# Kernel tuning notes

Hardware: AMD Instinct MI355X
Metric: run time of the kernel (lower is better)

The kernel has to match this reference:

```python
import jax, jax.numpy as jnp
import numpy as np

REG_LAMBDA = 0.1   # registration_lambda
EPS = 1e-8         # kornia convert_points_from_homogeneous eps


def angle_axis_to_rotation_matrix(aa):
    # aa: [B,3] angle-axis -> [B,3,3] rotation via Rodrigues formula
    theta2 = jnp.sum(aa * aa, axis=-1)                      # [B]
    theta = jnp.sqrt(theta2 + 1e-12)
    wx, wy, wz = aa[:, 0], aa[:, 1], aa[:, 2]
    z = jnp.zeros_like(wx)
    K = jnp.stack([z, -wz, wy, wz, z, -wx, -wy, wx, z], axis=-1).reshape(-1, 3, 3)
    A = (jnp.sin(theta) / theta)[:, None, None]
    B = ((1.0 - jnp.cos(theta)) / (theta2 + 1e-12))[:, None, None]
    I = jnp.eye(3, dtype=aa.dtype)
    return I + A * K + B * (K @ K)


def generate_transformation(position, angle):
    # [B,3],[B,3] -> [B,4,4] SE(3)
    R = angle_axis_to_rotation_matrix(angle)
    b = position.shape[0]
    top = jnp.concatenate([R, position[:, :, None]], axis=2)                      # [B,3,4]
    bottom = jnp.broadcast_to(jnp.array([0., 0., 0., 1.], dtype=position.dtype), (b, 1, 4))
    return jnp.concatenate([top, bottom], axis=1)


def generate_relative_transformation(pos_a, ang_a, pos_b, ang_b):
    Ta = generate_transformation(pos_a, ang_a)
    Tb = generate_transformation(pos_b, ang_b)
    return jnp.linalg.inv(Tb) @ Ta


def grid_sample_bilinear_zeros(img, xn, yn):
    # img: [B,C,H,W]; xn,yn: [B,H,W] in [-1,1]; align_corners=True, zeros padding
    B, C, H, W = img.shape
    ix = (xn + 1.0) * (W - 1) * 0.5
    iy = (yn + 1.0) * (H - 1) * 0.5
    x0 = jnp.floor(ix)
    y0 = jnp.floor(iy)
    wx1 = ix - x0
    wy1 = iy - y0

    def tap(xf, yf, w):
        valid = (xf >= 0) & (xf <= W - 1) & (yf >= 0) & (yf <= H - 1)
        xi = jnp.clip(xf, 0, W - 1).astype(jnp.int32)
        yi = jnp.clip(yf, 0, H - 1).astype(jnp.int32)
        vals = jax.vmap(lambda im, yy, xx: im[:, yy, xx])(img, yi, xi)  # [B,C,H,W]
        return vals * (w * valid)[:, None, :, :]

    return (tap(x0, y0, (1 - wx1) * (1 - wy1))
            + tap(x0 + 1, y0, wx1 * (1 - wy1))
            + tap(x0, y0 + 1, (1 - wx1) * wy1)
            + tap(x0 + 1, y0 + 1, wx1 * wy1))


def warp_frame_depth(image_src, depth_dst, src_trans_dst, K):
    # kornia.geometry.depth.warp_frame_depth
    B, C, H, W = image_src.shape
    u = jnp.arange(W, dtype=image_src.dtype)
    v = jnp.arange(H, dtype=image_src.dtype)
    uu, vv = jnp.meshgrid(u, v, indexing='xy')               # each [H,W]
    pix = jnp.stack([uu, vv, jnp.ones_like(uu)], axis=0)     # [3,H,W]
    rays = jnp.einsum('ij,jhw->ihw', jnp.linalg.inv(K), pix)  # unproject directions
    pts_dst = depth_dst * rays[None]                         # [B,3,H,W] 3D points in dst frame
    R = src_trans_dst[:, :3, :3]
    t = src_trans_dst[:, :3, 3]
    pts_src = jnp.einsum('bij,bjhw->bihw', R, pts_dst) + t[:, :, None, None]
    proj = jnp.einsum('ij,bjhw->bihw', K, pts_src)           # project to src pixels
    z = proj[:, 2]
    scale = jnp.where(jnp.abs(z) > EPS, 1.0 / z, jnp.ones_like(z))
    x = proj[:, 0] * scale
    y = proj[:, 1] * scale
    xn = 2.0 * x / (W - 1) - 1.0                             # normalize_pixel_coordinates
    yn = 2.0 * y / (H - 1) - 1.0
    return grid_sample_bilinear_zeros(image_src, xn, yn)


def setup_inputs() -> dict:
    key = jax.random.key(0)
    ks = jax.random.split(key, 6)
    B, H, W = 16, 384, 1280
    current_depth = jax.random.uniform(ks[0], (B, 1, H, W), jnp.float32) * 50.0 + 1.0
    next_depth = jax.random.uniform(ks[1], (B, 1, H, W), jnp.float32) * 50.0 + 1.0
    current_position = jax.random.normal(ks[2], (B, 3), jnp.float32) * 0.5
    next_position = jax.random.normal(ks[3], (B, 3), jnp.float32) * 0.5
    current_angle = jax.random.normal(ks[4], (B, 3), jnp.float32) * 0.05
    next_angle = jax.random.normal(ks[5], (B, 3), jnp.float32) * 0.05
    camera_matrix = jnp.array([[707.0912, 0.0, 640.0],
                               [0.0, 707.0912, 192.0],
                               [0.0, 0.0, 1.0]], dtype=jnp.float32)
    return {"current_depth": current_depth, "next_depth": next_depth,
            "current_position": current_position, "next_position": next_position,
            "current_angle": current_angle, "next_angle": next_angle,
            "camera_matrix": camera_matrix}


def reference(current_depth, next_depth, current_position, next_position,
              current_angle, next_angle, camera_matrix):
    T_c2n = generate_relative_transformation(current_position, current_angle,
                                             next_position, next_angle)
    T_n2c = generate_relative_transformation(next_position, next_angle,
                                             current_position, current_angle)
    generated_next_depth = warp_frame_depth(current_depth, next_depth, T_n2c, camera_matrix)
    generated_current_depth = warp_frame_depth(next_depth, current_depth, T_c2n, camera_matrix)
    loss_previous = jnp.mean(jnp.abs(generated_current_depth - current_depth))
    loss_next = jnp.mean(jnp.abs(generated_next_depth - next_depth))
    return (loss_previous + loss_next) / 2.0 * REG_LAMBDA
```

## Files before the change

kernel.cpp:

```cpp
#include <hip/hip_runtime.h>
#include <math.h>

constexpr int B = 16, H = 384, W = 1280;
constexpr int HW = H * W;
constexpr int NPIX = B * HW;
constexpr int HW4 = HW / 4;
constexpr int W4 = W / 4;
constexpr int NBLOCKS = 2048;
constexpr int NTHREADS = 256;
constexpr int NXCD = 8;
constexpr int BLK_PER_XCD = NBLOCKS / NXCD;
constexpr int THR_PER_XCD = BLK_PER_XCD * NTHREADS;
constexpr float EPSV = 1e-8f;

constexpr int PARAMS_FLOATS = B * 24;

__device__ inline void aa_to_R(float x, float y, float z, float R[9]) {
    float t2 = x * x + y * y + z * z;
    float th = sqrtf(t2 + 1e-12f);
    float A = sinf(th) / th;
    float Bc = (1.0f - cosf(th)) / (t2 + 1e-12f);
    R[0] = 1.0f + Bc * (-(y * y + z * z));
    R[1] = A * (-z) + Bc * (x * y);
    R[2] = A * ( y) + Bc * (x * z);
    R[3] = A * ( z) + Bc * (x * y);
    R[4] = 1.0f + Bc * (-(x * x + z * z));
    R[5] = A * (-x) + Bc * (y * z);
    R[6] = A * (-y) + Bc * (x * z);
    R[7] = A * ( x) + Bc * (y * z);
    R[8] = 1.0f + Bc * (-(x * x + y * y));
}

__device__ inline void mat3_mul(const float* A, const float* Bm, float* C) {
#pragma unroll
    for (int i = 0; i < 3; i++)
#pragma unroll
        for (int j = 0; j < 3; j++)
            C[i * 3 + j] = A[i * 3 + 0] * Bm[0 * 3 + j]
                         + A[i * 3 + 1] * Bm[1 * 3 + j]
                         + A[i * 3 + 2] * Bm[2 * 3 + j];
}

__device__ inline void compute_dir(const float Ra[9], const float Rb[9],
                                   const float ta[3], const float tb[3],
                                   const float K[9], const float Ki[9],
                                   float* out) {
    float Rrel[9];
#pragma unroll
    for (int i = 0; i < 3; i++)
#pragma unroll
        for (int j = 0; j < 3; j++)
            Rrel[i * 3 + j] = Ra[0 * 3 + i] * Rb[0 * 3 + j]
                            + Ra[1 * 3 + i] * Rb[1 * 3 + j]
                            + Ra[2 * 3 + i] * Rb[2 * 3 + j];
    float dt[3] = { tb[0] - ta[0], tb[1] - ta[1], tb[2] - ta[2] };
    float trel[3];
#pragma unroll
    for (int i = 0; i < 3; i++)
        trel[i] = Ra[0 * 3 + i] * dt[0] + Ra[1 * 3 + i] * dt[1] + Ra[2 * 3 + i] * dt[2];
    float tmp[9], M[9];
    mat3_mul(Rrel, Ki, tmp);
    mat3_mul(K, tmp, M);
#pragma unroll
    for (int i = 0; i < 9; i++) out[i] = M[i];
#pragma unroll
    for (int i = 0; i < 3; i++)
        out[9 + i] = K[i * 3 + 0] * trel[0] + K[i * 3 + 1] * trel[1] + K[i * 3 + 2] * trel[2];
}

__global__ void grl_setup_kernel(const float* __restrict__ cpos, const float* __restrict__ npos,
                                 const float* __restrict__ cang, const float* __restrict__ nang,
                                 const float* __restrict__ Kmat, float* __restrict__ ws) {
    int b = threadIdx.x;
    if (b >= B) return;
    float Rc[9], Rn[9];
    aa_to_R(cang[3 * b + 0], cang[3 * b + 1], cang[3 * b + 2], Rc);
    aa_to_R(nang[3 * b + 0], nang[3 * b + 1], nang[3 * b + 2], Rn);
    float tc[3] = { cpos[3 * b + 0], cpos[3 * b + 1], cpos[3 * b + 2] };
    float tn[3] = { npos[3 * b + 0], npos[3 * b + 1], npos[3 * b + 2] };
    float K[9];
#pragma unroll
    for (int i = 0; i < 9; i++) K[i] = Kmat[i];
    float det = K[0] * (K[4] * K[8] - K[5] * K[7])
              - K[1] * (K[3] * K[8] - K[5] * K[6])
              + K[2] * (K[3] * K[7] - K[4] * K[6]);
    float id = 1.0f / det;
    float Ki[9] = {
        (K[4] * K[8] - K[5] * K[7]) * id, (K[2] * K[7] - K[1] * K[8]) * id, (K[1] * K[5] - K[2] * K[4]) * id,
        (K[5] * K[6] - K[3] * K[8]) * id, (K[0] * K[8] - K[2] * K[6]) * id, (K[2] * K[3] - K[0] * K[5]) * id,
        (K[3] * K[7] - K[4] * K[6]) * id, (K[1] * K[6] - K[0] * K[7]) * id, (K[0] * K[4] - K[1] * K[3]) * id };
    float* out = ws + b * 24;
    compute_dir(Rc, Rn, tc, tn, K, Ki, out);
    compute_dir(Rn, Rc, tn, tc, K, Ki, out + 12);
}

__device__ inline float2 load2u(const float* __restrict__ p) {
    float2 v;
    __builtin_memcpy(&v, p, sizeof(float2));
    return v;
}

__global__ __launch_bounds__(NTHREADS, 4) void grl_warp_loss_kernel(
        const float* __restrict__ cur, const float* __restrict__ nxt,
        const float* __restrict__ ws, float* __restrict__ partials) {
    int bid = blockIdx.x;
    int xcd = bid & (NXCD - 1);
    int j   = bid >> 3;
    int tid0 = j * NTHREADS + (int)threadIdx.x;
    float sum = 0.0f;

    for (int bb = 0; bb < 2; ++bb) {
        int b = xcd * 2 + bb;
        const float* __restrict__ prm = ws + b * 24;
        float M[2][9], kt[2][3];
#pragma unroll
        for (int i = 0; i < 9; i++) { M[0][i] = prm[i]; M[1][i] = prm[12 + i]; }
#pragma unroll
        for (int i = 0; i < 3; i++) { kt[0][i] = prm[9 + i]; kt[1][i] = prm[21 + i]; }
        const float* __restrict__ srcimg[2];
        srcimg[0] = cur + b * HW;
        srcimg[1] = nxt + b * HW;

        for (int idx = tid0; idx < HW4; idx += THR_PER_XCD) {
            int h  = idx / W4;
            int w4 = idx - h * W4;
            int p  = idx * 4;
            const float4 c4 = *(const float4*)(srcimg[0] + p);
            const float4 n4 = *(const float4*)(srcimg[1] + p);
            float fh = (float)h;
            float dst[2][4] = { { n4.x, n4.y, n4.z, n4.w },
                                { c4.x, c4.y, c4.z, c4.w } };

            float2 pv[2][4][2];
            float  mxl[2][4], mxr[2][4];
            float  myt[2][4], myb[2][4];
            int    sL[2][4], sR[2][4];

#pragma unroll
            for (int dir = 0; dir < 2; dir++) {
                float rx = M[dir][1] * fh + M[dir][2];
                float ry = M[dir][4] * fh + M[dir][5];
                float rz = M[dir][7] * fh + M[dir][8];
#pragma unroll
                for (int k = 0; k < 4; k++) {
                    float fw = (float)(w4 * 4 + k);
                    float d  = dst[dir][k];
                    float px = d * (M[dir][0] * fw + rx) + kt[dir][0];
                    float py = d * (M[dir][3] * fw + ry) + kt[dir][1];
                    float pz = d * (M[dir][6] * fw + rz) + kt[dir][2];
                    float scale = (fabsf(pz) > EPSV) ? (1.0f / pz) : 1.0f;
                    float ix = px * scale, iy = py * scale;
                    float x0f = floorf(ix), y0f = floorf(iy);
                    float wx1 = ix - x0f, wy1 = iy - y0f;
                    float wx0 = 1.0f - wx1, wy0 = 1.0f - wy1;
                    bool vx0 = (x0f >= 0.0f)        & (x0f <= (float)(W - 1));
                    bool vx1 = (x0f + 1.0f >= 0.0f) & (x0f + 1.0f <= (float)(W - 1));
                    bool vy0 = (y0f >= 0.0f)        & (y0f <= (float)(H - 1));
                    bool vy1 = (y0f + 1.0f >= 0.0f) & (y0f + 1.0f <= (float)(H - 1));
                    mxl[dir][k] = vx0 ? wx0 : 0.0f;
                    mxr[dir][k] = vx1 ? wx1 : 0.0f;
                    myt[dir][k] = vy0 ? wy0 : 0.0f;
                    myb[dir][k] = vy1 ? wy1 : 0.0f;
                    int xi0 = (int)fminf(fmaxf(x0f,        0.0f), (float)(W - 1));
                    int xi1 = (int)fminf(fmaxf(x0f + 1.0f, 0.0f), (float)(W - 1));
                    int yi0 = (int)fminf(fmaxf(y0f,        0.0f), (float)(H - 1));
                    int yi1 = (int)fminf(fmaxf(y0f + 1.0f, 0.0f), (float)(H - 1));
                    int xp  = min(xi0, W - 2);
                    sL[dir][k] = xi0 - xp;
                    sR[dir][k] = xi1 - xp;
                    pv[dir][k][0] = load2u(srcimg[dir] + yi0 * W + xp);
                    pv[dir][k][1] = load2u(srcimg[dir] + yi1 * W + xp);
                }
            }
            __builtin_amdgcn_sched_barrier(0);
#pragma unroll
            for (int dir = 0; dir < 2; dir++)
#pragma unroll
                for (int k = 0; k < 4; k++) {
                    float2 p0 = pv[dir][k][0], p1 = pv[dir][k][1];
                    float v00 = sL[dir][k] ? p0.y : p0.x;
                    float v01 = sR[dir][k] ? p0.y : p0.x;
                    float v10 = sL[dir][k] ? p1.y : p1.x;
                    float v11 = sR[dir][k] ? p1.y : p1.x;
                    float acc = (v00 * mxl[dir][k] + v01 * mxr[dir][k]) * myt[dir][k]
                              + (v10 * mxl[dir][k] + v11 * mxr[dir][k]) * myb[dir][k];
                    sum += fabsf(acc - dst[dir][k]);
                }
        }
    }

#pragma unroll
    for (int off2 = 32; off2 > 0; off2 >>= 1) sum += __shfl_down(sum, off2, 64);
    __shared__ float smem[NTHREADS / 64];
    int lane = threadIdx.x & 63, wid = threadIdx.x >> 6;
    if (lane == 0) smem[wid] = sum;
    __syncthreads();
    if (threadIdx.x == 0) {
        float t = 0.0f;
#pragma unroll
        for (int i = 0; i < NTHREADS / 64; i++) t += smem[i];
        partials[blockIdx.x] = t;
    }
}

__global__ __launch_bounds__(256) void grl_finalize_kernel(const float* __restrict__ partials,
                                                           float* __restrict__ out) {
    float sum = 0.0f;
    for (int i = threadIdx.x; i < NBLOCKS; i += 256) sum += partials[i];
#pragma unroll
    for (int off = 32; off > 0; off >>= 1) sum += __shfl_down(sum, off, 64);
    __shared__ float smem[4];
    int lane = threadIdx.x & 63, wid = threadIdx.x >> 6;
    if (lane == 0) smem[wid] = sum;
    __syncthreads();
    if (threadIdx.x == 0) {
        float t = smem[0] + smem[1] + smem[2] + smem[3];
        out[0] = t * (0.1f / (2.0f * (float)NPIX));
    }
}

extern "C" void kernel_launch(void* const* d_in, const int* in_sizes, int n_in,
                              void* d_out, int out_size, void* d_ws, size_t ws_size,
                              hipStream_t stream) {
    const float* cur  = (const float*)d_in[0];
    const float* nxt  = (const float*)d_in[1];
    const float* cpos = (const float*)d_in[2];
    const float* npos = (const float*)d_in[3];
    const float* cang = (const float*)d_in[4];
    const float* nang = (const float*)d_in[5];
    const float* Kmat = (const float*)d_in[6];
    float* ws = (float*)d_ws;
    float* partials = ws + PARAMS_FLOATS;

    grl_setup_kernel<<<1, 64, 0, stream>>>(cpos, npos, cang, nang, Kmat, ws);
    grl_warp_loss_kernel<<<NBLOCKS, NTHREADS, 0, stream>>>(cur, nxt, ws, partials);
    grl_finalize_kernel<<<1, 256, 0, stream>>>(partials, (float*)d_out);
}
```

Baseline: 116.9 us.

## Software-pipeline gather loads across flattened tasks with two in-flight stages

Merges the two per-XCD batch loops into one flat task space and unrolls it into a fixed sequence of issue/consume stages, so one stage's gather loads are outstanding while the previous stage is reduced. The bilinear x-select is folded into four precomputed tap coefficients, which removes the per-tap selects. Launch bounds drop to two blocks per SIMD to leave room for the doubled register staging. The trade-off is lower occupancy and an unrolled schedule that assumes at most four tasks per thread, which holds for the fixed sizes.

```diff
diff --git a/kernel.cpp b/kernel.cpp
--- a/kernel.cpp
+++ b/kernel.cpp
@@ -11,6 +11,7 @@
 constexpr int NXCD = 8;
 constexpr int BLK_PER_XCD = NBLOCKS / NXCD;
 constexpr int THR_PER_XCD = BLK_PER_XCD * NTHREADS;
+constexpr int NTASK = 2 * HW4;
 constexpr float EPSV = 1e-8f;
 
 constexpr int PARAMS_FLOATS = B * 24;
@@ -100,7 +101,92 @@
     return v;
 }
 
-__global__ __launch_bounds__(NTHREADS, 4) void grl_warp_loss_kernel(
+struct Stage {
+    float2 p0[8], p1[8];
+    float  c00[8], c01[8], c10[8], c11[8];
+    float  dst[8];
+};
+
+__device__ inline void issue_stage(int t, int xcd,
+                                   const float* __restrict__ cur,
+                                   const float* __restrict__ nxt,
+                                   const float* __restrict__ ws, Stage& S) {
+    int bl  = (t >= HW4) ? 1 : 0;
+    int idx = t - bl * HW4;
+    int b   = xcd * 2 + bl;
+    const float* __restrict__ prm = ws + b * 24;
+    const float* __restrict__ img0 = cur + b * HW;
+    const float* __restrict__ img1 = nxt + b * HW;
+    int h  = idx / W4;
+    int w4 = idx - h * W4;
+    int p  = idx * 4;
+    const float4 c4 = *(const float4*)(img0 + p);
+    const float4 n4 = *(const float4*)(img1 + p);
+    float fh = (float)h;
+    float dstv[2][4] = { { n4.x, n4.y, n4.z, n4.w },
+                         { c4.x, c4.y, c4.z, c4.w } };
+#pragma unroll
+    for (int dir = 0; dir < 2; dir++) {
+        const float* __restrict__ img = dir ? img1 : img0;
+        float M0 = prm[dir * 12 + 0], M1 = prm[dir * 12 + 1], M2 = prm[dir * 12 + 2];
+        float M3 = prm[dir * 12 + 3], M4 = prm[dir * 12 + 4], M5 = prm[dir * 12 + 5];
+        float M6 = prm[dir * 12 + 6], M7 = prm[dir * 12 + 7], M8 = prm[dir * 12 + 8];
+        float k0 = prm[dir * 12 + 9], k1 = prm[dir * 12 + 10], k2 = prm[dir * 12 + 11];
+        float rx = M1 * fh + M2;
+        float ry = M4 * fh + M5;
+        float rz = M7 * fh + M8;
+#pragma unroll
+        for (int k = 0; k < 4; k++) {
+            int i = dir * 4 + k;
+            float fw = (float)(w4 * 4 + k);
+            float d  = dstv[dir][k];
+            float px = d * (M0 * fw + rx) + k0;
+            float py = d * (M3 * fw + ry) + k1;
+            float pz = d * (M6 * fw + rz) + k2;
+            float scale = (fabsf(pz) > EPSV) ? (1.0f / pz) : 1.0f;
+            float ix = px * scale, iy = py * scale;
+            float x0f = floorf(ix), y0f = floorf(iy);
+            float wx1 = ix - x0f, wy1 = iy - y0f;
+            float wx0 = 1.0f - wx1, wy0 = 1.0f - wy1;
+            bool vx0 = (x0f >= 0.0f)        & (x0f <= (float)(W - 1));
+            bool vx1 = (x0f + 1.0f >= 0.0f) & (x0f + 1.0f <= (float)(W - 1));
+            bool vy0 = (y0f >= 0.0f)        & (y0f <= (float)(H - 1));
+            bool vy1 = (y0f + 1.0f >= 0.0f) & (y0f + 1.0f <= (float)(H - 1));
+            float mxl = vx0 ? wx0 : 0.0f;
+            float mxr = vx1 ? wx1 : 0.0f;
+            float myt = vy0 ? wy0 : 0.0f;
+            float myb = vy1 ? wy1 : 0.0f;
+            int xi0 = (int)fminf(fmaxf(x0f,        0.0f), (float)(W - 1));
+            int xi1 = (int)fminf(fmaxf(x0f + 1.0f, 0.0f), (float)(W - 1));
+            int yi0 = (int)fminf(fmaxf(y0f,        0.0f), (float)(H - 1));
+            int yi1 = (int)fminf(fmaxf(y0f + 1.0f, 0.0f), (float)(H - 1));
+            int xp  = min(xi0, W - 2);
+            int sL = xi0 - xp, sR = xi1 - xp;
+            float ax = (sL ? 0.0f : mxl) + (sR ? 0.0f : mxr);
+            float bx = (sL ? mxl : 0.0f) + (sR ? mxr : 0.0f);
+            S.c00[i] = ax * myt;
+            S.c01[i] = bx * myt;
+            S.c10[i] = ax * myb;
+            S.c11[i] = bx * myb;
+            S.dst[i] = d;
+            S.p0[i] = load2u(img + yi0 * W + xp);
+            S.p1[i] = load2u(img + yi1 * W + xp);
+        }
+    }
+}
+
+__device__ inline float consume_stage(const Stage& S) {
+    float s = 0.0f;
+#pragma unroll
+    for (int i = 0; i < 8; i++) {
+        float g = S.p0[i].x * S.c00[i] + S.p0[i].y * S.c01[i]
+                + S.p1[i].x * S.c10[i] + S.p1[i].y * S.c11[i];
+        s += fabsf(g - S.dst[i]);
+    }
+    return s;
+}
+
+__global__ __launch_bounds__(NTHREADS, 2) void grl_warp_loss_kernel(
         const float* __restrict__ cur, const float* __restrict__ nxt,
         const float* __restrict__ ws, float* __restrict__ partials) {
     int bid = blockIdx.x;
@@ -109,84 +195,22 @@
     int tid0 = j * NTHREADS + (int)threadIdx.x;
     float sum = 0.0f;
 
-    for (int bb = 0; bb < 2; ++bb) {
-        int b = xcd * 2 + bb;
-        const float* __restrict__ prm = ws + b * 24;
-        float M[2][9], kt[2][3];
-#pragma unroll
-        for (int i = 0; i < 9; i++) { M[0][i] = prm[i]; M[1][i] = prm[12 + i]; }
-#pragma unroll
-        for (int i = 0; i < 3; i++) { kt[0][i] = prm[9 + i]; kt[1][i] = prm[21 + i]; }
-        const float* __restrict__ srcimg[2];
-        srcimg[0] = cur + b * HW;
-        srcimg[1] = nxt + b * HW;
-
-        for (int idx = tid0; idx < HW4; idx += THR_PER_XCD) {
-            int h  = idx / W4;
-            int w4 = idx - h * W4;
-            int p  = idx * 4;
-            const float4 c4 = *(const float4*)(srcimg[0] + p);
-            const float4 n4 = *(const float4*)(srcimg[1] + p);
-            float fh = (float)h;
-            float dst[2][4] = { { n4.x, n4.y, n4.z, n4.w },
-                                { c4.x, c4.y, c4.z, c4.w } };
-
-            float2 pv[2][4][2];
-            float  mxl[2][4], mxr[2][4];
-            float  myt[2][4], myb[2][4];
-            int    sL[2][4], sR[2][4];
-
-#pragma unroll
-            for (int dir = 0; dir < 2; dir++) {
-                float rx = M[dir][1] * fh + M[dir][2];
-                float ry = M[dir][4] * fh + M[dir][5];
-                float rz = M[dir][7] * fh + M[dir][8];
-#pragma unroll
-                for (int k = 0; k < 4; k++) {
-                    float fw = (float)(w4 * 4 + k);
-                    float d  = dst[dir][k];
-                    float px = d * (M[dir][0] * fw + rx) + kt[dir][0];
-                    float py = d * (M[dir][3] * fw + ry) + kt[dir][1];
-                    float pz = d * (M[dir][6] * fw + rz) + kt[dir][2];
-                    float scale = (fabsf(pz) > EPSV) ? (1.0f / pz) : 1.0f;
-                    float ix = px * scale, iy = py * scale;
-                    float x0f = floorf(ix), y0f = floorf(iy);
-                    float wx1 = ix - x0f, wy1 = iy - y0f;
-                    float wx0 = 1.0f - wx1, wy0 = 1.0f - wy1;
-                    bool vx0 = (x0f >= 0.0f)        & (x0f <= (float)(W - 1));
-                    bool vx1 = (x0f + 1.0f >= 0.0f) & (x0f + 1.0f <= (float)(W - 1));
-                    bool vy0 = (y0f >= 0.0f)        & (y0f <= (float)(H - 1));
-                    bool vy1 = (y0f + 1.0f >= 0.0f) & (y0f + 1.0f <= (float)(H - 1));
-                    mxl[dir][k] = vx0 ? wx0 : 0.0f;
-                    mxr[dir][k] = vx1 ? wx1 : 0.0f;
-                    myt[dir][k] = vy0 ? wy0 : 0.0f;
-                    myb[dir][k] = vy1 ? wy1 : 0.0f;
-                    int xi0 = (int)fminf(fmaxf(x0f,        0.0f), (float)(W - 1));
-                    int xi1 = (int)fminf(fmaxf(x0f + 1.0f, 0.0f), (float)(W - 1));
-                    int yi0 = (int)fminf(fmaxf(y0f,        0.0f), (float)(H - 1));
-                    int yi1 = (int)fminf(fmaxf(y0f + 1.0f, 0.0f), (float)(H - 1));
-                    int xp  = min(xi0, W - 2);
-                    sL[dir][k] = xi0 - xp;
-                    sR[dir][k] = xi1 - xp;
-                    pv[dir][k][0] = load2u(srcimg[dir] + yi0 * W + xp);
-                    pv[dir][k][1] = load2u(srcimg[dir] + yi1 * W + xp);
-                }
-            }
-            __builtin_amdgcn_sched_barrier(0);
-#pragma unroll
-            for (int dir = 0; dir < 2; dir++)
-#pragma unroll
-                for (int k = 0; k < 4; k++) {
-                    float2 p0 = pv[dir][k][0], p1 = pv[dir][k][1];
-                    float v00 = sL[dir][k] ? p0.y : p0.x;
-                    float v01 = sR[dir][k] ? p0.y : p0.x;
-                    float v10 = sL[dir][k] ? p1.y : p1.x;
-                    float v11 = sR[dir][k] ? p1.y : p1.x;
-                    float acc = (v00 * mxl[dir][k] + v01 * mxr[dir][k]) * myt[dir][k]
-                              + (v10 * mxl[dir][k] + v11 * mxr[dir][k]) * myb[dir][k];
-                    sum += fabsf(acc - dst[dir][k]);
-                }
-        }
+    Stage A, Bs;
+    issue_stage(tid0,                 xcd, cur, nxt, ws, A);
+    issue_stage(tid0 + THR_PER_XCD,   xcd, cur, nxt, ws, Bs);
+    __builtin_amdgcn_sched_barrier(0);
+    sum += consume_stage(A);
+    issue_stage(tid0 + 2 * THR_PER_XCD, xcd, cur, nxt, ws, A);
+    __builtin_amdgcn_sched_barrier(0);
+    sum += consume_stage(Bs);
+    int t3 = tid0 + 3 * THR_PER_XCD;
+    if (t3 < NTASK) {
+        issue_stage(t3, xcd, cur, nxt, ws, Bs);
+        __builtin_amdgcn_sched_barrier(0);
+        sum += consume_stage(A);
+        sum += consume_stage(Bs);
+    } else {
+        sum += consume_stage(A);
     }
 
 #pragma unroll
```

Result: slower. 125.6 us (+7.4%).

## Process eight pixels per thread and precombine bilinear weights before gathers

Applied to the files above, without the earlier changes.

Each thread now handles eight consecutive pixels instead of four, so twice as many gather loads are issued before the scheduling barrier. The hope is that more memory-level parallelism hides gather latency. The select-based tap choice is replaced by four precomputed coefficients per pixel, leaving a plain four-term dot product after the loads. The extra live registers lower the launch-bounds occupancy hint from 4 to 3, which cuts the number of waves available to hide latency.

```diff
diff --git a/kernel.cpp b/kernel.cpp
--- a/kernel.cpp
+++ b/kernel.cpp
@@ -4,8 +4,8 @@
 constexpr int B = 16, H = 384, W = 1280;
 constexpr int HW = H * W;
 constexpr int NPIX = B * HW;
-constexpr int HW4 = HW / 4;
-constexpr int W4 = W / 4;
+constexpr int HW8 = HW / 8;
+constexpr int W8 = W / 8;
 constexpr int NBLOCKS = 2048;
 constexpr int NTHREADS = 256;
 constexpr int NXCD = 8;
@@ -100,7 +100,7 @@
     return v;
 }
 
-__global__ __launch_bounds__(NTHREADS, 4) void grl_warp_loss_kernel(
+__global__ __launch_bounds__(NTHREADS, 3) void grl_warp_loss_kernel(
         const float* __restrict__ cur, const float* __restrict__ nxt,
         const float* __restrict__ ws, float* __restrict__ partials) {
     int bid = blockIdx.x;
@@ -121,20 +121,20 @@
         srcimg[0] = cur + b * HW;
         srcimg[1] = nxt + b * HW;
 
-        for (int idx = tid0; idx < HW4; idx += THR_PER_XCD) {
-            int h  = idx / W4;
-            int w4 = idx - h * W4;
-            int p  = idx * 4;
-            const float4 c4 = *(const float4*)(srcimg[0] + p);
-            const float4 n4 = *(const float4*)(srcimg[1] + p);
+        for (int idx = tid0; idx < HW8; idx += THR_PER_XCD) {
+            int h  = idx / W8;
+            int w8 = idx - h * W8;
+            int p  = idx * 8;
+            const float4 c4a = *(const float4*)(srcimg[0] + p);
+            const float4 c4b = *(const float4*)(srcimg[0] + p + 4);
+            const float4 n4a = *(const float4*)(srcimg[1] + p);
+            const float4 n4b = *(const float4*)(srcimg[1] + p + 4);
             float fh = (float)h;
-            float dst[2][4] = { { n4.x, n4.y, n4.z, n4.w },
-                                { c4.x, c4.y, c4.z, c4.w } };
-
-            float2 pv[2][4][2];
-            float  mxl[2][4], mxr[2][4];
-            float  myt[2][4], myb[2][4];
-            int    sL[2][4], sR[2][4];
+            float dst[2][8] = { { n4a.x, n4a.y, n4a.z, n4a.w, n4b.x, n4b.y, n4b.z, n4b.w },
+                                { c4a.x, c4a.y, c4a.z, c4a.w, c4b.x, c4b.y, c4b.z, c4b.w } };
+
+            float2 pv0[2][8], pv1[2][8];
+            float  c00[2][8], c01[2][8], c10[2][8], c11[2][8];
 
 #pragma unroll
             for (int dir = 0; dir < 2; dir++) {
@@ -142,8 +142,8 @@
                 float ry = M[dir][4] * fh + M[dir][5];
                 float rz = M[dir][7] * fh + M[dir][8];
 #pragma unroll
-                for (int k = 0; k < 4; k++) {
-                    float fw = (float)(w4 * 4 + k);
+                for (int k = 0; k < 8; k++) {
+                    float fw = (float)(w8 * 8 + k);
                     float d  = dst[dir][k];
                     float px = d * (M[dir][0] * fw + rx) + kt[dir][0];
                     float py = d * (M[dir][3] * fw + ry) + kt[dir][1];
@@ -157,34 +157,34 @@
                     bool vx1 = (x0f + 1.0f >= 0.0f) & (x0f + 1.0f <= (float)(W - 1));
                     bool vy0 = (y0f >= 0.0f)        & (y0f <= (float)(H - 1));
                     bool vy1 = (y0f + 1.0f >= 0.0f) & (y0f + 1.0f <= (float)(H - 1));
-                    mxl[dir][k] = vx0 ? wx0 : 0.0f;
-                    mxr[dir][k] = vx1 ? wx1 : 0.0f;
-                    myt[dir][k] = vy0 ? wy0 : 0.0f;
-                    myb[dir][k] = vy1 ? wy1 : 0.0f;
+                    float mxl = vx0 ? wx0 : 0.0f;
+                    float mxr = vx1 ? wx1 : 0.0f;
+                    float myt = vy0 ? wy0 : 0.0f;
+                    float myb = vy1 ? wy1 : 0.0f;
                     int xi0 = (int)fminf(fmaxf(x0f,        0.0f), (float)(W - 1));
                     int xi1 = (int)fminf(fmaxf(x0f + 1.0f, 0.0f), (float)(W - 1));
                     int yi0 = (int)fminf(fmaxf(y0f,        0.0f), (float)(H - 1));
                     int yi1 = (int)fminf(fmaxf(y0f + 1.0f, 0.0f), (float)(H - 1));
                     int xp  = min(xi0, W - 2);
-                    sL[dir][k] = xi0 - xp;
-                    sR[dir][k] = xi1 - xp;
-                    pv[dir][k][0] = load2u(srcimg[dir] + yi0 * W + xp);
-                    pv[dir][k][1] = load2u(srcimg[dir] + yi1 * W + xp);
+                    int sL = xi0 - xp, sR = xi1 - xp;
+                    float ax = (sL ? 0.0f : mxl) + (sR ? 0.0f : mxr);
+                    float bx = (sL ? mxl : 0.0f) + (sR ? mxr : 0.0f);
+                    c00[dir][k] = ax * myt;
+                    c01[dir][k] = bx * myt;
+                    c10[dir][k] = ax * myb;
+                    c11[dir][k] = bx * myb;
+                    pv0[dir][k] = load2u(srcimg[dir] + yi0 * W + xp);
+                    pv1[dir][k] = load2u(srcimg[dir] + yi1 * W + xp);
                 }
             }
             __builtin_amdgcn_sched_barrier(0);
 #pragma unroll
             for (int dir = 0; dir < 2; dir++)
 #pragma unroll
-                for (int k = 0; k < 4; k++) {
-                    float2 p0 = pv[dir][k][0], p1 = pv[dir][k][1];
-                    float v00 = sL[dir][k] ? p0.y : p0.x;
-                    float v01 = sR[dir][k] ? p0.y : p0.x;
-                    float v10 = sL[dir][k] ? p1.y : p1.x;
-                    float v11 = sR[dir][k] ? p1.y : p1.x;
-                    float acc = (v00 * mxl[dir][k] + v01 * mxr[dir][k]) * myt[dir][k]
-                              + (v10 * mxl[dir][k] + v11 * mxr[dir][k]) * myb[dir][k];
-                    sum += fabsf(acc - dst[dir][k]);
+                for (int k = 0; k < 8; k++) {
+                    float g = pv0[dir][k].x * c00[dir][k] + pv0[dir][k].y * c01[dir][k]
+                            + pv1[dir][k].x * c10[dir][k] + pv1[dir][k].y * c11[dir][k];
+                    sum += fabsf(g - dst[dir][k]);
                 }
         }
     }
```

Result: slower. 132.8 us (+13.6%).
